# Performance work log

Hardware: AMD Instinct MI355X
Metric: run time of the kernel (lower is better)

Reference implementation:

```python
import jax, jax.numpy as jnp
import numpy as np

T, B = 2048, 32
LIS, SPE, ATT = 1024, 1024, 512


def setup_inputs() -> dict:
    key = jax.random.key(0)
    ks = jax.random.split(key, 10)
    s = 0.02
    return {
        "listener_state": jax.random.normal(ks[0], (T, B, LIS), jnp.float32),
        "speller_state": jax.random.normal(ks[1], (B, SPE), jnp.float32),
        "listener_len": jax.random.randint(ks[2], (B,), 1, T + 1),
        "batch_size": B,
        "W_score": jax.random.normal(ks[3], (LIS, ATT), jnp.float32) * s,
        "b_score": jnp.zeros((ATT,), jnp.float32),
        "W_value": jax.random.normal(ks[4], (LIS, ATT), jnp.float32) * s,
        "b_value": jnp.zeros((ATT,), jnp.float32),
        "W_proj": jax.random.normal(ks[5], (SPE, ATT), jnp.float32) * s,
        "b_proj": jnp.zeros((ATT,), jnp.float32),
    }


def reference(listener_state, speller_state, listener_len, batch_size,
              W_score, b_score, W_value, b_value, W_proj, b_proj):
    # batch_first=False path: [T,B,D] -> [B,T,D]
    x = jnp.transpose(listener_state, (1, 0, 2))
    keys = jax.nn.relu(x @ W_score + b_score)          # [B,T,A]
    vals = jax.nn.relu(x @ W_value + b_value)          # [B,T,A]
    query = jax.nn.relu(speller_state @ W_proj + b_proj)  # [B,A]
    scores = jnp.einsum('ba,bta->bt', query, keys)     # [B,T]
    # vectorized length mask: additive -100 past valid length (faithful to source)
    t = jnp.arange(keys.shape[1])
    mask = jnp.where(t[None, :] >= listener_len[:, None], -100.0, 0.0)
    attn = jax.nn.softmax(scores + mask, axis=1)       # [B,T]
    context = jnp.einsum('bt,bta->ba', attn, vals)     # [B,A]
    return (context, attn)
```

## Files before the change

kernel.cpp:

```cpp
#include <hip/hip_runtime.h>
#include <hip/hip_bf16.h>
#include <hip/hip_fp16.h>

#define T_DIM 2048
#define B_DIM 32
#define LIS_DIM 1024
#define SPE_DIM 1024
#define ATT_DIM 512

typedef _Float16 f16x8 __attribute__((ext_vector_type(8)));
typedef _Float16 f16x4 __attribute__((ext_vector_type(4)));
typedef float f32x4 __attribute__((ext_vector_type(4)));
typedef float f32x16 __attribute__((ext_vector_type(16)));
typedef unsigned int u32;

__global__ __launch_bounds__(256)
void prep_kernel(const float* __restrict__ Ws, const float* __restrict__ Wv,
                 _Float16* __restrict__ WTf, const float* __restrict__ spe,
                 const float* __restrict__ Wp, const float* __restrict__ bp,
                 float* __restrict__ q, float* __restrict__ scores) {
  int p = blockIdx.x, tid = threadIdx.x;
  if (p < 64) {
    __shared__ float wlds[64 * 257];
    int nb = p >> 4, c = p & 15;
    const float* W = (nb >> 1) ? Wv : Ws;
    int col0 = (nb & 1) * 256;
    for (int i = 0; i < 64; ++i) {
      int e = i * 256 + tid;
      int r = e >> 8, cl = e & 255;
      wlds[r * 257 + cl] = W[(size_t)(c * 64 + r) * ATT_DIM + col0 + cl];
    }
    __syncthreads();
    int lane = tid & 63, ks = tid >> 6, hk = lane >> 5, cs = lane & 31;
#pragma unroll
    for (int ct = 0; ct < 8; ++ct) {
      f16x8 h;
#pragma unroll
      for (int jj = 0; jj < 8; ++jj)
        h[jj] = (_Float16)wlds[(ks * 16 + hk * 8 + jj) * 257 + ct * 32 + cs];
      ((f16x8*)WTf)[(size_t)(((p * 4 + ks) * 8 + ct)) * 64 + lane] = h;
    }
  } else if (p < 96) {
    __shared__ float s[SPE_DIM];
    int b = p - 64;
    for (int i = tid; i < SPE_DIM; i += 256) s[i] = spe[(size_t)b * SPE_DIM + i];
    __syncthreads();
    for (int a = tid; a < ATT_DIM; a += 256) {
      float acc = bp[a];
      for (int l = 0; l < SPE_DIM; ++l)
        acc = fmaf(s[l], Wp[(size_t)l * ATT_DIM + a], acc);
      q[(size_t)b * ATT_DIM + a] = fmaxf(acc, 0.f);
    }
  } else {
    int base = (p - 96) * 8192;
    for (int i = 0; i < 32; ++i) scores[base + i * 256 + tid] = 0.f;
  }
}

__global__ __launch_bounds__(512, 2)
void gemm_kernel(const float* __restrict__ x, const _Float16* __restrict__ WTf,
                 const float* __restrict__ bs, const float* __restrict__ bv,
                 const float* __restrict__ q, float* __restrict__ scores,
                 _Float16* __restrict__ vals_p) {
  __shared__ __align__(16) _Float16 A_lds[2][16384];
  __shared__ __align__(16) _Float16 W_lds[2][16384];
  __shared__ float bias_s[256], q_s[256], red_s[256];

  const int tid = threadIdx.x;
  const int raw = blockIdx.x;
  const int xcd = raw & 7;
  const int j   = raw >> 3;
  const int nb  = j & 3;
  const int tile = (j >> 2) * 8 + xcd;
  const int b   = tile >> 3;
  const int tm  = tile & 7;
  const int t0  = tm * 256;
  const bool is_scores = (nb < 2);

  const float* bias_src = is_scores ? (bs + (nb & 1) * 256) : (bv + (nb & 1) * 256);
  if (tid < 256) {
    bias_s[tid] = bias_src[tid];
    red_s[tid] = 0.f;
    if (is_scores) q_s[tid] = q[(size_t)b * ATT_DIM + nb * 256 + tid];
  }

  const int wv = tid >> 6, lane = tid & 63;
  const int wr = wv >> 2, wc = wv & 3;
  const int ts = lane & 31, hk = lane >> 5;

  const float* xb = x + (size_t)b * LIS_DIM;
  f32x4 sl[8];
  auto stage_load = [&](int c) {
#pragma unroll
    for (int i = 0; i < 8; ++i) {
      int e = i * 512 + tid;
      int row = e >> 4, q4 = e & 15;
      sl[i] = *((const f32x4*)(xb + (size_t)(t0 + row) * (B_DIM * LIS_DIM) + c * 64) + q4);
    }
  };
  auto stage_write = [&](int bufi) {
    char* buf = (char*)A_lds[bufi];
#pragma unroll
    for (int i = 0; i < 8; ++i) {
      int e = i * 512 + tid;
      int row = e >> 4, q4 = e & 15;
      f16x4 h;
      h[0] = (_Float16)sl[i][0]; h[1] = (_Float16)sl[i][1];
      h[2] = (_Float16)sl[i][2]; h[3] = (_Float16)sl[i][3];
      *(f16x4*)(buf + row * 128 + ((q4 * 8) ^ ((row & 7) << 4))) = h;
    }
  };
  auto w_prefetch = [&](int c, int bufi) {
    const char* slice = (const char*)WTf + ((size_t)(nb * 16 + c)) * 32768;
    char* lb = (char*)W_lds[bufi] + wv * 1024;
#pragma unroll
    for (int i = 0; i < 4; ++i) {
      __builtin_amdgcn_global_load_lds(
          (const __attribute__((address_space(1))) u32*)(slice + i * 8192 + tid * 16),
          (__attribute__((address_space(3))) u32*)(lb + i * 8192), 16, 0, 0);
    }
  };

  f32x16 acc[4][2];
#pragma unroll
  for (int m = 0; m < 4; ++m)
#pragma unroll
    for (int n = 0; n < 2; ++n)
      acc[m][n] = (f32x16)(0.f);

  w_prefetch(0, 0);
  stage_load(0);
  stage_write(0);
  asm volatile("s_waitcnt vmcnt(0) lgkmcnt(0)" ::: "memory");
  __builtin_amdgcn_s_barrier();

  for (int c = 0; c < 16; ++c) {
    const int bi = c & 1;
    if (c < 15) { w_prefetch(c + 1, bi ^ 1); stage_load(c + 1); }
    const char* Ab = (const char*)A_lds[bi];
    const char* Wb = (const char*)W_lds[bi];
#pragma unroll
    for (int ks = 0; ks < 4; ++ks) {
      f16x8 wf[2], bx[4];
#pragma unroll
      for (int n = 0; n < 2; ++n)
        wf[n] = *(const f16x8*)(Wb + (ks * 8 + wc * 2 + n) * 1024 + lane * 16);
#pragma unroll
      for (int m = 0; m < 4; ++m) {
        int row = wr * 128 + m * 32 + ts;
        bx[m] = *(const f16x8*)(Ab + row * 128 + ((ks * 32 + hk * 16) ^ ((row & 7) << 4)));
      }
      __builtin_amdgcn_s_setprio(1);
#pragma unroll
      for (int n = 0; n < 2; ++n)
#pragma unroll
        for (int m = 0; m < 4; ++m)
          acc[m][n] = __builtin_amdgcn_mfma_f32_32x32x16_f16(wf[n], bx[m], acc[m][n], 0, 0, 0);
      __builtin_amdgcn_s_setprio(0);
    }
    if (c < 15) stage_write(bi ^ 1);
    asm volatile("s_waitcnt vmcnt(0) lgkmcnt(0)" ::: "memory");
    __builtin_amdgcn_s_barrier();
  }

  if (is_scores) {
#pragma unroll
    for (int m = 0; m < 4; ++m) {
      float s = 0.f;
#pragma unroll
      for (int n = 0; n < 2; ++n)
#pragma unroll
        for (int rg = 0; rg < 16; ++rg) {
          int cl = wc * 64 + n * 32 + (rg & 3) + 8 * (rg >> 2) + 4 * hk;
          s += q_s[cl] * fmaxf(acc[m][n][rg] + bias_s[cl], 0.f);
        }
      s += __shfl_xor(s, 32, 64);
      if (lane < 32) atomicAdd(&red_s[wr * 128 + m * 32 + ts], s);
    }
    __syncthreads();
    if (tid < 256) atomicAdd(&scores[(size_t)b * T_DIM + t0 + tid], red_s[tid]);
  } else {
    _Float16* vb = vals_p + (((size_t)tile * 2 + (nb - 2)) * 8 + wv) * 8192;
#pragma unroll
    for (int m = 0; m < 4; ++m)
#pragma unroll
      for (int n = 0; n < 2; ++n)
#pragma unroll
        for (int g = 0; g < 4; ++g) {
          f16x4 h;
#pragma unroll
          for (int r = 0; r < 4; ++r) {
            int cl = wc * 64 + n * 32 + 8 * g + 4 * hk + r;
            h[r] = (_Float16)fmaxf(acc[m][n][g * 4 + r] + bias_s[cl], 0.f);
          }
          *(f16x4*)(vb + (size_t)(((m * 2 + n) * 4 + g) * 64 + lane) * 4) = h;
        }
  }
}

__global__ void softmax_kernel(const float* __restrict__ scores,
                               const int* __restrict__ llen,
                               float* __restrict__ attn_out) {
  __shared__ float rmax[4], rsum[4];
  int b = blockIdx.x, tid = threadIdx.x;
  int L = llen[b];
  float v[8];
  float mx = -1e30f;
  for (int i = 0; i < 8; ++i) {
    int t = i * 256 + tid;
    float s = scores[(size_t)b * T_DIM + t];
    if (t >= L) s -= 100.f;
    v[i] = s;
    mx = fmaxf(mx, s);
  }
  for (int d = 1; d < 64; d <<= 1) mx = fmaxf(mx, __shfl_xor(mx, d, 64));
  if ((tid & 63) == 0) rmax[tid >> 6] = mx;
  __syncthreads();
  mx = fmaxf(fmaxf(rmax[0], rmax[1]), fmaxf(rmax[2], rmax[3]));
  float sum = 0.f;
  for (int i = 0; i < 8; ++i) { v[i] = expf(v[i] - mx); sum += v[i]; }
  for (int d = 1; d < 64; d <<= 1) sum += __shfl_xor(sum, d, 64);
  if ((tid & 63) == 0) rsum[tid >> 6] = sum;
  __syncthreads();
  sum = rsum[0] + rsum[1] + rsum[2] + rsum[3];
  float inv = 1.f / sum;
  for (int i = 0; i < 8; ++i)
    attn_out[(size_t)b * T_DIM + i * 256 + tid] = v[i] * inv;
}

__global__ __launch_bounds__(512)
void ctx_kernel(const _Float16* __restrict__ vals_p,
                const float* __restrict__ attn,
                float* __restrict__ ctx) {
  __shared__ float attn_s[T_DIM];
  int blk = blockIdx.x;
  int b = blk >> 1, nb2 = blk & 1;
  int tid = threadIdx.x;
#pragma unroll
  for (int i = 0; i < 4; ++i)
    attn_s[i * 512 + tid] = attn[(size_t)b * T_DIM + i * 512 + tid];
  __syncthreads();
  int w = tid >> 6, L = tid & 63;
  int wc = w >> 1, n = w & 1, h = L >> 5, ts = L & 31;
  float acc[4][4] = {};
  for (int tm = 0; tm < 8; ++tm) {
    int tile = b * 8 + tm;
#pragma unroll
    for (int wr = 0; wr < 2; ++wr) {
      const _Float16* base = vals_p + (((size_t)tile * 2 + nb2) * 8 + (wr * 4 + wc)) * 8192;
#pragma unroll
      for (int m = 0; m < 4; ++m) {
        float a = attn_s[tm * 256 + wr * 128 + m * 32 + ts];
#pragma unroll
        for (int g = 0; g < 4; ++g) {
          f16x4 v = *(const f16x4*)(base + (size_t)(((m * 2 + n) * 4 + g) * 64 + L) * 4);
#pragma unroll
          for (int r = 0; r < 4; ++r) acc[g][r] += a * (float)v[r];
        }
      }
    }
  }
#pragma unroll
  for (int g = 0; g < 4; ++g)
#pragma unroll
    for (int r = 0; r < 4; ++r) {
      float v2 = acc[g][r];
      v2 += __shfl_xor(v2, 1, 64);
      v2 += __shfl_xor(v2, 2, 64);
      v2 += __shfl_xor(v2, 4, 64);
      v2 += __shfl_xor(v2, 8, 64);
      v2 += __shfl_xor(v2, 16, 64);
      if (ts == 0)
        ctx[(size_t)b * ATT_DIM + nb2 * 256 + wc * 64 + n * 32 + 8 * g + 4 * h + r] = v2;
    }
}

extern "C" void kernel_launch(void* const* d_in, const int* in_sizes, int n_in,
                              void* d_out, int out_size, void* d_ws, size_t ws_size,
                              hipStream_t stream) {
  const float* x   = (const float*)d_in[0];
  const float* spe = (const float*)d_in[1];
  const int*   len = (const int*)d_in[2];
  const float* Ws  = (const float*)d_in[4];
  const float* bs  = (const float*)d_in[5];
  const float* Wv  = (const float*)d_in[6];
  const float* bv  = (const float*)d_in[7];
  const float* Wp  = (const float*)d_in[8];
  const float* bp  = (const float*)d_in[9];
  float* out = (float*)d_out;

  char* ws = (char*)d_ws;
  _Float16* WTf  = (_Float16*)ws;
  float* q       = (float*)(ws + (2u << 20));
  float* scores  = (float*)(ws + (2u << 20) + (64u << 10));
  _Float16* vals = (_Float16*)(ws + (4u << 20));

  prep_kernel<<<dim3(104), dim3(256), 0, stream>>>(Ws, Wv, WTf, spe, Wp, bp, q, scores);
  gemm_kernel<<<dim3(1024), dim3(512), 0, stream>>>(x, WTf, bs, bv, q, scores, vals);
  softmax_kernel<<<dim3(32), dim3(256), 0, stream>>>(scores, len, out + 16384);
  ctx_kernel<<<dim3(64), dim3(512), 0, stream>>>(vals, out + 16384, out);
}
```

Before: 298.3 us.

## Retile GEMM to 128-row tiles with 32-wide K steps and triple-buffered weights

Measured after the change: 286.4 us. 1.04x faster.

```diff
diff --git a/kernel.cpp b/kernel.cpp
--- a/kernel.cpp
+++ b/kernel.cpp
@@ -32,13 +32,14 @@
     }
     __syncthreads();
     int lane = tid & 63, ks = tid >> 6, hk = lane >> 5, cs = lane & 31;
+    int c5 = 2 * c + (ks >> 1), ks2 = ks & 1;
 #pragma unroll
     for (int ct = 0; ct < 8; ++ct) {
       f16x8 h;
 #pragma unroll
       for (int jj = 0; jj < 8; ++jj)
         h[jj] = (_Float16)wlds[(ks * 16 + hk * 8 + jj) * 257 + ct * 32 + cs];
-      ((f16x8*)WTf)[(size_t)(((p * 4 + ks) * 8 + ct)) * 64 + lane] = h;
+      ((f16x8*)WTf)[(size_t)(((nb * 32 + c5) * 2 + ks2) * 8 + ct) * 64 + lane] = h;
     }
   } else if (p < 96) {
     __shared__ float s[SPE_DIM];
@@ -57,14 +58,14 @@
   }
 }
 
-__global__ __launch_bounds__(512, 2)
+__global__ __launch_bounds__(256, 2)
 void gemm_kernel(const float* __restrict__ x, const _Float16* __restrict__ WTf,
                  const float* __restrict__ bs, const float* __restrict__ bv,
                  const float* __restrict__ q, float* __restrict__ scores,
                  _Float16* __restrict__ vals_p) {
-  __shared__ __align__(16) _Float16 A_lds[2][16384];
-  __shared__ __align__(16) _Float16 W_lds[2][16384];
-  __shared__ float bias_s[256], q_s[256], red_s[256];
+  __shared__ __align__(16) char A_lds[2][10240];
+  __shared__ __align__(16) char W_lds[3][16384];
+  __shared__ float bias_s[256], q_s[256], red_s[128];
 
   const int tid = threadIdx.x;
   const int raw = blockIdx.x;
@@ -72,53 +73,48 @@
   const int j   = raw >> 3;
   const int nb  = j & 3;
   const int tile = (j >> 2) * 8 + xcd;
-  const int b   = tile >> 3;
-  const int tm  = tile & 7;
-  const int t0  = tm * 256;
+  const int b   = tile >> 4;
+  const int tm  = tile & 15;
+  const int t0  = tm * 128;
   const bool is_scores = (nb < 2);
 
-  const float* bias_src = is_scores ? (bs + (nb & 1) * 256) : (bv + (nb & 1) * 256);
-  if (tid < 256) {
-    bias_s[tid] = bias_src[tid];
-    red_s[tid] = 0.f;
-    if (is_scores) q_s[tid] = q[(size_t)b * ATT_DIM + nb * 256 + tid];
-  }
+  bias_s[tid] = is_scores ? bs[(nb & 1) * 256 + tid] : bv[(nb - 2) * 256 + tid];
+  if (is_scores) q_s[tid] = q[(size_t)b * ATT_DIM + nb * 256 + tid];
+  if (tid < 128) red_s[tid] = 0.f;
 
   const int wv = tid >> 6, lane = tid & 63;
-  const int wr = wv >> 2, wc = wv & 3;
   const int ts = lane & 31, hk = lane >> 5;
 
   const float* xb = x + (size_t)b * LIS_DIM;
-  f32x4 sl[8];
+  f32x4 sl[4];
   auto stage_load = [&](int c) {
 #pragma unroll
-    for (int i = 0; i < 8; ++i) {
-      int e = i * 512 + tid;
-      int row = e >> 4, q4 = e & 15;
-      sl[i] = *((const f32x4*)(xb + (size_t)(t0 + row) * (B_DIM * LIS_DIM) + c * 64) + q4);
+    for (int i = 0; i < 4; ++i) {
+      int e = i * 256 + tid;
+      int row = e >> 3, q4 = e & 7;
+      sl[i] = *((const f32x4*)(xb + (size_t)(t0 + row) * (B_DIM * LIS_DIM) + c * 32) + q4);
     }
   };
   auto stage_write = [&](int bufi) {
-    char* buf = (char*)A_lds[bufi];
-#pragma unroll
-    for (int i = 0; i < 8; ++i) {
-      int e = i * 512 + tid;
-      int row = e >> 4, q4 = e & 15;
+    char* buf = A_lds[bufi];
+#pragma unroll
+    for (int i = 0; i < 4; ++i) {
+      int e = i * 256 + tid;
+      int row = e >> 3, q4 = e & 7;
       f16x4 h;
       h[0] = (_Float16)sl[i][0]; h[1] = (_Float16)sl[i][1];
       h[2] = (_Float16)sl[i][2]; h[3] = (_Float16)sl[i][3];
-      *(f16x4*)(buf + row * 128 + ((q4 * 8) ^ ((row & 7) << 4))) = h;
+      *(f16x4*)(buf + row * 80 + q4 * 8) = h;
     }
   };
   auto w_prefetch = [&](int c, int bufi) {
-    const char* slice = (const char*)WTf + ((size_t)(nb * 16 + c)) * 32768;
-    char* lb = (char*)W_lds[bufi] + wv * 1024;
-#pragma unroll
-    for (int i = 0; i < 4; ++i) {
+    const char* slice = (const char*)WTf + (size_t)(nb * 32 + c) * 16384;
+    char* lb = W_lds[bufi] + wv * 1024;
+#pragma unroll
+    for (int i = 0; i < 4; ++i)
       __builtin_amdgcn_global_load_lds(
-          (const __attribute__((address_space(1))) u32*)(slice + i * 8192 + tid * 16),
-          (__attribute__((address_space(3))) u32*)(lb + i * 8192), 16, 0, 0);
-    }
+          (const __attribute__((address_space(1))) u32*)(slice + i * 4096 + tid * 16),
+          (__attribute__((address_space(3))) u32*)(lb + i * 4096), 16, 0, 0);
   };
 
   f32x16 acc[4][2];
@@ -131,24 +127,30 @@
   w_prefetch(0, 0);
   stage_load(0);
   stage_write(0);
-  asm volatile("s_waitcnt vmcnt(0) lgkmcnt(0)" ::: "memory");
+  w_prefetch(1, 1);
+  asm volatile("s_waitcnt lgkmcnt(0)" ::: "memory");
   __builtin_amdgcn_s_barrier();
 
-  for (int c = 0; c < 16; ++c) {
+  int wb = 0;
+  for (int c = 0; c < 32; ++c) {
     const int bi = c & 1;
-    if (c < 15) { w_prefetch(c + 1, bi ^ 1); stage_load(c + 1); }
-    const char* Ab = (const char*)A_lds[bi];
-    const char* Wb = (const char*)W_lds[bi];
-#pragma unroll
-    for (int ks = 0; ks < 4; ++ks) {
+    if (c < 31) stage_load(c + 1);
+    if (c < 30) {
+      int wt = wb + 2; if (wt >= 3) wt -= 3;
+      w_prefetch(c + 2, wt);
+    }
+    const char* Ab = A_lds[bi];
+    const char* Wb = W_lds[wb];
+#pragma unroll
+    for (int ks = 0; ks < 2; ++ks) {
       f16x8 wf[2], bx[4];
 #pragma unroll
       for (int n = 0; n < 2; ++n)
-        wf[n] = *(const f16x8*)(Wb + (ks * 8 + wc * 2 + n) * 1024 + lane * 16);
+        wf[n] = *(const f16x8*)(Wb + (ks * 8 + wv * 2 + n) * 1024 + lane * 16);
 #pragma unroll
       for (int m = 0; m < 4; ++m) {
-        int row = wr * 128 + m * 32 + ts;
-        bx[m] = *(const f16x8*)(Ab + row * 128 + ((ks * 32 + hk * 16) ^ ((row & 7) << 4)));
+        int row = m * 32 + ts;
+        bx[m] = *(const f16x8*)(Ab + row * 80 + ks * 32 + hk * 16);
       }
       __builtin_amdgcn_s_setprio(1);
 #pragma unroll
@@ -158,9 +160,10 @@
           acc[m][n] = __builtin_amdgcn_mfma_f32_32x32x16_f16(wf[n], bx[m], acc[m][n], 0, 0, 0);
       __builtin_amdgcn_s_setprio(0);
     }
-    if (c < 15) stage_write(bi ^ 1);
-    asm volatile("s_waitcnt vmcnt(0) lgkmcnt(0)" ::: "memory");
+    if (c < 31) stage_write(bi ^ 1);
+    asm volatile("s_waitcnt lgkmcnt(0)" ::: "memory");
     __builtin_amdgcn_s_barrier();
+    ++wb; if (wb == 3) wb = 0;
   }
 
   if (is_scores) {
@@ -171,16 +174,16 @@
       for (int n = 0; n < 2; ++n)
 #pragma unroll
         for (int rg = 0; rg < 16; ++rg) {
-          int cl = wc * 64 + n * 32 + (rg & 3) + 8 * (rg >> 2) + 4 * hk;
+          int cl = wv * 64 + n * 32 + (rg & 3) + 8 * (rg >> 2) + 4 * hk;
           s += q_s[cl] * fmaxf(acc[m][n][rg] + bias_s[cl], 0.f);
         }
       s += __shfl_xor(s, 32, 64);
-      if (lane < 32) atomicAdd(&red_s[wr * 128 + m * 32 + ts], s);
+      if (lane < 32) atomicAdd(&red_s[m * 32 + ts], s);
     }
     __syncthreads();
-    if (tid < 256) atomicAdd(&scores[(size_t)b * T_DIM + t0 + tid], red_s[tid]);
+    if (tid < 128) atomicAdd(&scores[(size_t)b * T_DIM + t0 + tid], red_s[tid]);
   } else {
-    _Float16* vb = vals_p + (((size_t)tile * 2 + (nb - 2)) * 8 + wv) * 8192;
+    _Float16* vb = vals_p + ((size_t)(tile * 2 + (nb - 2)) * 4 + wv) * 8192;
 #pragma unroll
     for (int m = 0; m < 4; ++m)
 #pragma unroll
@@ -190,10 +193,11 @@
           f16x4 h;
 #pragma unroll
           for (int r = 0; r < 4; ++r) {
-            int cl = wc * 64 + n * 32 + 8 * g + 4 * hk + r;
+            int cl = wv * 64 + n * 32 + 8 * g + 4 * hk + r;
             h[r] = (_Float16)fmaxf(acc[m][n][g * 4 + r] + bias_s[cl], 0.f);
           }
-          *(f16x4*)(vb + (size_t)(((m * 2 + n) * 4 + g) * 64 + lane) * 4) = h;
+          __builtin_nontemporal_store(
+              h, (f16x4*)(vb + (size_t)(((m * 2 + n) * 4 + g) * 64 + lane) * 4));
         }
   }
 }
@@ -233,46 +237,52 @@
                 const float* __restrict__ attn,
                 float* __restrict__ ctx) {
   __shared__ float attn_s[T_DIM];
+  __shared__ float red[256];
   int blk = blockIdx.x;
   int b = blk >> 1, nb2 = blk & 1;
   int tid = threadIdx.x;
 #pragma unroll
   for (int i = 0; i < 4; ++i)
     attn_s[i * 512 + tid] = attn[(size_t)b * T_DIM + i * 512 + tid];
+  if (tid < 256) red[tid] = 0.f;
   __syncthreads();
-  int w = tid >> 6, L = tid & 63;
-  int wc = w >> 1, n = w & 1, h = L >> 5, ts = L & 31;
-  float acc[4][4] = {};
-  for (int tm = 0; tm < 8; ++tm) {
-    int tile = b * 8 + tm;
-#pragma unroll
-    for (int wr = 0; wr < 2; ++wr) {
-      const _Float16* base = vals_p + (((size_t)tile * 2 + nb2) * 8 + (wr * 4 + wc)) * 8192;
-#pragma unroll
-      for (int m = 0; m < 4; ++m) {
-        float a = attn_s[tm * 256 + wr * 128 + m * 32 + ts];
+  int wave = tid >> 6, lane = tid & 63;
+  int w = wave >> 1, half = wave & 1, ts = lane & 31, hk = lane >> 5;
+  float a2[2][4][4] = {};
+  for (int t8 = 0; t8 < 8; ++t8) {
+    int tm = half * 8 + t8;
+    int tile = b * 16 + tm;
+    const _Float16* base = vals_p + ((size_t)(tile * 2 + nb2) * 4 + w) * 8192;
+#pragma unroll
+    for (int m = 0; m < 4; ++m) {
+      float a = attn_s[tm * 128 + m * 32 + ts];
+#pragma unroll
+      for (int n = 0; n < 2; ++n)
 #pragma unroll
         for (int g = 0; g < 4; ++g) {
-          f16x4 v = *(const f16x4*)(base + (size_t)(((m * 2 + n) * 4 + g) * 64 + L) * 4);
-#pragma unroll
-          for (int r = 0; r < 4; ++r) acc[g][r] += a * (float)v[r];
+          f16x4 v = __builtin_nontemporal_load(
+              (const f16x4*)(base + (size_t)(((m * 2 + n) * 4 + g) * 64 + lane) * 4));
+#pragma unroll
+          for (int r = 0; r < 4; ++r) a2[n][g][r] += a * (float)v[r];
         }
+    }
+  }
+#pragma unroll
+  for (int n = 0; n < 2; ++n)
+#pragma unroll
+    for (int g = 0; g < 4; ++g)
+#pragma unroll
+      for (int r = 0; r < 4; ++r) {
+        float v2 = a2[n][g][r];
+        v2 += __shfl_xor(v2, 1, 64);
+        v2 += __shfl_xor(v2, 2, 64);
+        v2 += __shfl_xor(v2, 4, 64);
+        v2 += __shfl_xor(v2, 8, 64);
+        v2 += __shfl_xor(v2, 16, 64);
+        if (ts == 0) atomicAdd(&red[w * 64 + n * 32 + 8 * g + 4 * hk + r], v2);
       }
-    }
-  }
-#pragma unroll
-  for (int g = 0; g < 4; ++g)
-#pragma unroll
-    for (int r = 0; r < 4; ++r) {
-      float v2 = acc[g][r];
-      v2 += __shfl_xor(v2, 1, 64);
-      v2 += __shfl_xor(v2, 2, 64);
-      v2 += __shfl_xor(v2, 4, 64);
-      v2 += __shfl_xor(v2, 8, 64);
-      v2 += __shfl_xor(v2, 16, 64);
-      if (ts == 0)
-        ctx[(size_t)b * ATT_DIM + nb2 * 256 + wc * 64 + n * 32 + 8 * g + 4 * h + r] = v2;
-    }
+  __syncthreads();
+  if (tid < 256) ctx[(size_t)b * ATT_DIM + nb2 * 256 + tid] = red[tid];
 }
 
 extern "C" void kernel_launch(void* const* d_in, const int* in_sizes, int n_in,
@@ -296,7 +306,7 @@
   _Float16* vals = (_Float16*)(ws + (4u << 20));
 
   prep_kernel<<<dim3(104), dim3(256), 0, stream>>>(Ws, Wv, WTf, spe, Wp, bp, q, scores);
-  gemm_kernel<<<dim3(1024), dim3(512), 0, stream>>>(x, WTf, bs, bv, q, scores, vals);
+  gemm_kernel<<<dim3(2048), dim3(256), 0, stream>>>(x, WTf, bs, bv, q, scores, vals);
   softmax_kernel<<<dim3(32), dim3(256), 0, stream>>>(scores, len, out + 16384);
   ctx_kernel<<<dim3(64), dim3(512), 0, stream>>>(vals, out + 16384, out);
 }
```
